# Kernel optimization log

Measured on AMD Instinct MI355X. Metric: run time of the kernel, lower is better.

The kernel has to match this reference:

```python
import jax, jax.numpy as jnp
import numpy as np

N, D, K = 100000, 512, 32
H1, H2 = 512, 256
LN2PI_2 = float(np.log(2.0 * np.pi) / 2.0)


def _glorot(key, shape):
    fan_in, fan_out = shape[0], shape[1]
    limit = np.sqrt(6.0 / (fan_in + fan_out))
    return jax.random.uniform(key, shape, jnp.float32, -limit, limit)


def setup_inputs() -> dict:
    key = jax.random.key(0)
    k0, k1, k2, k3 = jax.random.split(key, 4)
    return {
        "x": jax.random.normal(k0, (N, D), jnp.float32),
        "W1": _glorot(k1, (D, H1)),
        "b1": jnp.zeros((H1,), jnp.float32),
        "W2": _glorot(k2, (H1, H2)),
        "b2": jnp.zeros((H2,), jnp.float32),
        "W3": _glorot(k3, (H2, K)),
        "b3": jnp.zeros((K,), jnp.float32),
    }


def reference(x, W1, b1, W2, b2, W3, b3):
    # instance attention MLP: softplus hiddens, softmax output -> [N, K]
    h = jax.nn.softplus(x @ W1 + b1)
    h = jax.nn.softplus(h @ W2 + b2)
    att = jax.nn.softmax(h @ W3 + b3, axis=-1)

    att_sum = jnp.sum(att, axis=0)  # [K]
    # weighted mean: sum_n x[n,d] * att[n,k] / sum_n att[n,k]  -> [K, D]
    means = (att.T @ x) / att_sum[:, None]
    # weighted variance: E_w[x^2] - mean^2 (algebraic expansion of
    # sum_n (x - mean)^2 * att / sum att, avoids [N,K,D] intermediate)
    ex2 = (att.T @ (x * x)) / att_sum[:, None]  # [K, D]
    vars_ = ex2 - means * means

    # GMM diagonal log-likelihood, expanded to GEMM form:
    inv_v = 1.0 / vars_  # [K, D]
    maha = (x * x) @ inv_v.T - 2.0 * (x @ (means * inv_v).T) \
           + jnp.sum(means * means * inv_v, axis=-1)[None, :]  # [N, K]
    gmm_log = -0.5 * maha - 0.5 * jnp.sum(jnp.log(vars_), axis=-1)[None, :] - D * LN2PI_2
    return gmm_log, vars_
```

## Files before the change

### kernel.cpp

```cpp
#include <hip/hip_runtime.h>
#include <hip/hip_bf16.h>
#include <math.h>

#define NROWS 100000
#define DDIM  512
#define KCL   32
#define H1DIM 512
#define H2DIM 256
#define LN2PI_2 0.9189385332046727f
#define NCHUNK 196
#define NPAD  100352
#define NBLK  784

typedef __attribute__((ext_vector_type(8))) short short8;
typedef __attribute__((ext_vector_type(4))) short shortx4;
typedef __attribute__((ext_vector_type(4))) float floatx4;

__device__ __forceinline__ float softplus_f(float v) {
    return fmaxf(v, 0.f) + __logf(1.f + __expf(-fabsf(v)));
}

__device__ __forceinline__ unsigned short f2bf_rne(float f) {
    unsigned int u = __float_as_uint(f);
    return (unsigned short)((u + 0x7fffu + ((u >> 16) & 1u)) >> 16);
}

__device__ __forceinline__ float bf2f(short v) {
    return __uint_as_float(((unsigned int)(unsigned short)v) << 16);
}

__device__ __forceinline__ short8 cvt8(float4 a, float4 b) {
    union { unsigned int u[4]; short8 s; } r;
    asm("v_cvt_pk_bf16_f32 %0, %1, %2" : "=v"(r.u[0]) : "v"(a.x), "v"(a.y));
    asm("v_cvt_pk_bf16_f32 %0, %1, %2" : "=v"(r.u[1]) : "v"(a.z), "v"(a.w));
    asm("v_cvt_pk_bf16_f32 %0, %1, %2" : "=v"(r.u[2]) : "v"(b.x), "v"(b.y));
    asm("v_cvt_pk_bf16_f32 %0, %1, %2" : "=v"(r.u[3]) : "v"(b.z), "v"(b.w));
    return r.s;
}

__global__ __launch_bounds__(256) void cvt_weights(
    const float* __restrict__ W1, const float* __restrict__ W2,
    const float* __restrict__ W3, short* __restrict__ W1T,
    short* __restrict__ W2T, short* __restrict__ W3T)
{
    int idx = blockIdx.x * 256 + threadIdx.x;
    const int n1 = DDIM * H1DIM;
    const int n2 = H1DIM * H2DIM;
    const int n3 = H2DIM * KCL;
    if (idx < n1) {
        int n = idx % H1DIM, k = idx / H1DIM;
        W1T[(size_t)n * DDIM + k] = (short)f2bf_rne(W1[idx]);
    } else if (idx < n1 + n2) {
        int rel = idx - n1;
        int n = rel % H2DIM, k = rel / H2DIM;
        W2T[(size_t)n * H1DIM + k] = (short)f2bf_rne(W2[rel]);
    } else if (idx < n1 + n2 + n3) {
        int rel = idx - n1 - n2;
        int n = rel % KCL, k = rel / KCL;
        W3T[(size_t)n * H2DIM + k] = (short)f2bf_rne(W3[rel]);
    }
}

#define LDP 40
template<int AFP32>
__global__ __launch_bounds__(256) void gemm_sp(
    const void* __restrict__ Aptr, const short* __restrict__ BT,
    const float* __restrict__ bias, void* __restrict__ Cptr,
    int M, int Nc, int Kd, int out_bf16)
{
    __shared__ short As[2][128 * LDP];
    __shared__ short Bs[2][128 * LDP];

    const int tid = threadIdx.x;
    const int lid = tid & 63;
    const int w = tid >> 6;
    const int lm = lid & 15;
    const int lq = lid >> 4;
    const int wrow = (w & 1) * 64;
    const int wcol = (w >> 1) * 64;

    const int nwg = gridDim.x * gridDim.y;
    const int bid = blockIdx.y * gridDim.x + blockIdx.x;
    const int q = nwg >> 3, r = nwg & 7;
    const int xcd = bid & 7, slot = bid >> 3;
    const int L = (xcd < r ? xcd * (q + 1) : r * (q + 1) + (xcd - r) * q) + slot;
    const int row0 = (L / gridDim.x) * 128;
    const int col0 = (L % gridDim.x) * 128;

    const int sr = tid >> 2;
    const int sc = (tid & 3) << 3;

    int gr0 = row0 + sr;       if (gr0 >= M) gr0 = M - 1;
    int gr1 = row0 + 64 + sr;  if (gr1 >= M) gr1 = M - 1;

    const float* Ar0f = (const float*)Aptr + (size_t)gr0 * Kd + sc;
    const float* Ar1f = (const float*)Aptr + (size_t)gr1 * Kd + sc;
    const short* Ar0s = (const short*)Aptr + (size_t)gr0 * Kd + sc;
    const short* Ar1s = (const short*)Aptr + (size_t)gr1 * Kd + sc;
    const short* Br0 = BT + (size_t)(col0 + sr) * Kd + sc;
    const short* Br1 = BT + (size_t)(col0 + 64 + sr) * Kd + sc;

    floatx4 acc[4][4];
    #pragma unroll
    for (int i = 0; i < 4; i++)
        #pragma unroll
        for (int j = 0; j < 4; j++)
            acc[i][j] = (floatx4){0.f, 0.f, 0.f, 0.f};

    float4 fa0, fa1, fa2, fa3;
    short8 pa0, pa1, pb0, pb1;
    if constexpr (AFP32) {
        fa0 = *(const float4*)Ar0f; fa1 = *(const float4*)(Ar0f + 4);
        fa2 = *(const float4*)Ar1f; fa3 = *(const float4*)(Ar1f + 4);
    } else {
        pa0 = *(const short8*)Ar0s;
        pa1 = *(const short8*)Ar1s;
    }
    pb0 = *(const short8*)Br0;
    pb1 = *(const short8*)Br1;

    const int nk = Kd >> 5;
    for (int kt = 0; kt < nk; kt++) {
        const int buf = kt & 1;
        if constexpr (AFP32) {
            *(short8*)&As[buf][sr * LDP + sc]        = cvt8(fa0, fa1);
            *(short8*)&As[buf][(64 + sr) * LDP + sc] = cvt8(fa2, fa3);
        } else {
            *(short8*)&As[buf][sr * LDP + sc]        = pa0;
            *(short8*)&As[buf][(64 + sr) * LDP + sc] = pa1;
        }
        *(short8*)&Bs[buf][sr * LDP + sc]        = pb0;
        *(short8*)&Bs[buf][(64 + sr) * LDP + sc] = pb1;
        if (kt + 1 < nk) {
            int ko = (kt + 1) << 5;
            if constexpr (AFP32) {
                fa0 = *(const float4*)(Ar0f + ko);
                fa1 = *(const float4*)(Ar0f + ko + 4);
                fa2 = *(const float4*)(Ar1f + ko);
                fa3 = *(const float4*)(Ar1f + ko + 4);
            } else {
                pa0 = *(const short8*)(Ar0s + ko);
                pa1 = *(const short8*)(Ar1s + ko);
            }
            pb0 = *(const short8*)(Br0 + ko);
            pb1 = *(const short8*)(Br1 + ko);
        }
        __syncthreads();

        short8 a[4], b[4];
        #pragma unroll
        for (int i = 0; i < 4; i++)
            a[i] = *(const short8*)&As[buf][(wrow + i * 16 + lm) * LDP + lq * 8];
        #pragma unroll
        for (int j = 0; j < 4; j++)
            b[j] = *(const short8*)&Bs[buf][(wcol + j * 16 + lm) * LDP + lq * 8];
        #pragma unroll
        for (int i = 0; i < 4; i++)
            #pragma unroll
            for (int j = 0; j < 4; j++)
                acc[i][j] = __builtin_amdgcn_mfma_f32_16x16x32_bf16(
                    a[i], b[j], acc[i][j], 0, 0, 0);
    }

    float bb[4];
    #pragma unroll
    for (int j = 0; j < 4; j++)
        bb[j] = bias[col0 + wcol + j * 16 + lm];

    #pragma unroll
    for (int i = 0; i < 4; i++) {
        #pragma unroll
        for (int reg = 0; reg < 4; reg++) {
            int rr = row0 + wrow + i * 16 + lq * 4 + reg;
            if (rr < M) {
                #pragma unroll
                for (int j = 0; j < 4; j++) {
                    int c = col0 + wcol + j * 16 + lm;
                    float v = softplus_f(acc[i][j][reg] + bb[j]);
                    if (out_bf16)
                        ((short*)Cptr)[(size_t)rr * Nc + c] = (short)f2bf_rne(v);
                    else
                        ((float*)Cptr)[(size_t)rr * Nc + c] = v;
                }
            }
        }
    }
}

__global__ __launch_bounds__(256) void logits_mfma(
    const short* __restrict__ h2b, const short* __restrict__ W3T,
    const float* __restrict__ b3, short* __restrict__ attT,
    float* __restrict__ Patt)
{
    __shared__ short Ts[32][136];
    __shared__ float red[4][32];

    const int tid = threadIdx.x;
    const int lane = tid & 63;
    const int lm = lane & 15;
    const int lq = lane >> 4;
    const int w = tid >> 6;
    const int wrow = w * 32;
    const int row0 = blockIdx.x * 128;

    short8 bf[2][8];
    #pragma unroll
    for (int j = 0; j < 2; j++)
        #pragma unroll
        for (int s = 0; s < 8; s++)
            bf[j][s] = *(const short8*)&W3T[(j * 16 + lm) * H2DIM + s * 32 + lq * 8];

    int gr0 = row0 + wrow + lm;      if (gr0 >= NROWS) gr0 = NROWS - 1;
    int gr1 = row0 + wrow + 16 + lm; if (gr1 >= NROWS) gr1 = NROWS - 1;
    const short* a0p = h2b + (size_t)gr0 * H2DIM + lq * 8;
    const short* a1p = h2b + (size_t)gr1 * H2DIM + lq * 8;

    floatx4 acc[2][2];
    #pragma unroll
    for (int i = 0; i < 2; i++)
        #pragma unroll
        for (int j = 0; j < 2; j++)
            acc[i][j] = (floatx4){0.f, 0.f, 0.f, 0.f};

    #pragma unroll
    for (int s = 0; s < 8; s++) {
        short8 a0 = *(const short8*)(a0p + s * 32);
        short8 a1 = *(const short8*)(a1p + s * 32);
        acc[0][0] = __builtin_amdgcn_mfma_f32_16x16x32_bf16(a0, bf[0][s], acc[0][0], 0, 0, 0);
        acc[0][1] = __builtin_amdgcn_mfma_f32_16x16x32_bf16(a0, bf[1][s], acc[0][1], 0, 0, 0);
        acc[1][0] = __builtin_amdgcn_mfma_f32_16x16x32_bf16(a1, bf[0][s], acc[1][0], 0, 0, 0);
        acc[1][1] = __builtin_amdgcn_mfma_f32_16x16x32_bf16(a1, bf[1][s], acc[1][1], 0, 0, 0);
    }

    const float b3v0 = b3[lm];
    const float b3v1 = b3[16 + lm];

    float p0 = 0.f, p1 = 0.f;

    #pragma unroll
    for (int i = 0; i < 2; i++) {
        #pragma unroll
        for (int reg = 0; reg < 4; reg++) {
            const int rloc = wrow + i * 16 + lq * 4 + reg;
            const int rg = row0 + rloc;
            float v0 = acc[i][0][reg] + b3v0;
            float v1 = acc[i][1][reg] + b3v1;
            float m = fmaxf(v0, v1);
            m = fmaxf(m, __shfl_xor(m, 1));
            m = fmaxf(m, __shfl_xor(m, 2));
            m = fmaxf(m, __shfl_xor(m, 4));
            m = fmaxf(m, __shfl_xor(m, 8));
            float e0 = __expf(v0 - m);
            float e1 = __expf(v1 - m);
            float sm = e0 + e1;
            sm += __shfl_xor(sm, 1);
            sm += __shfl_xor(sm, 2);
            sm += __shfl_xor(sm, 4);
            sm += __shfl_xor(sm, 8);
            float inv = 1.f / sm;
            e0 *= inv; e1 *= inv;
            if (rg >= NROWS) { e0 = 0.f; e1 = 0.f; }
            p0 += e0; p1 += e1;
            Ts[lm][rloc]      = (short)f2bf_rne(e0);
            Ts[16 + lm][rloc] = (short)f2bf_rne(e1);
        }
    }

    p0 += __shfl_xor(p0, 16); p0 += __shfl_xor(p0, 32);
    p1 += __shfl_xor(p1, 16); p1 += __shfl_xor(p1, 32);
    if (lq == 0) { red[w][lm] = p0; red[w][16 + lm] = p1; }

    __syncthreads();

    if (tid < KCL)
        Patt[blockIdx.x * KCL + tid] =
            red[0][tid] + red[1][tid] + red[2][tid] + red[3][tid];

    #pragma unroll
    for (int p = 0; p < 2; p++) {
        int u = p * 256 + tid;
        int rr = u >> 4;
        int cs = (u & 15) << 3;
        short8 o = *(const short8*)&Ts[rr][cs];
        *(short8*)&attT[(size_t)rr * NPAD + row0 + cs] = o;
    }
}

__global__ __launch_bounds__(256, 4) void stats_mfma(
    const float* __restrict__ x, const short* __restrict__ attT,
    float* __restrict__ P)
{
    __shared__ short xT[32 * 512];

    const int tid = threadIdx.x;
    const int lane = tid & 63;
    const int lm = lane & 15;
    const int lq = lane >> 4;
    const int w = tid >> 6;
    const int kh = w >> 1;
    const int dh = w & 1;

    const int cblk = blockIdx.x;
    const int dgrp = blockIdx.y;
    const int n0 = cblk * 512;

    short8 afrag[16];
    const short* arow = attT + (size_t)(kh * 16 + lm) * NPAD + n0 + lq * 8;
    #pragma unroll
    for (int s = 0; s < 16; s++)
        afrag[s] = *(const short8*)(arow + s * 32);

    const int c = tid & 31;
    const int rq = tid >> 5;
    const bool full = (n0 + 512 <= NROWS);

    for (int dt = 0; dt < 4; dt++) {
        const int colf = dgrp * 128 + dt * 32 + c;
        __syncthreads();
        if (full) {
            const float* xp = x + (size_t)n0 * DDIM + colf;
            #pragma unroll 4
            for (int p = 0; p < 16; p++) {
                int rr = p * 32 + rq * 4;
                float f0 = xp[(size_t)(rr + 0) * DDIM];
                float f1 = xp[(size_t)(rr + 1) * DDIM];
                float f2 = xp[(size_t)(rr + 2) * DDIM];
                float f3 = xp[(size_t)(rr + 3) * DDIM];
                unsigned int u01 = (unsigned int)f2bf_rne(f0) |
                                   ((unsigned int)f2bf_rne(f1) << 16);
                unsigned int u23 = (unsigned int)f2bf_rne(f2) |
                                   ((unsigned int)f2bf_rne(f3) << 16);
                int boff = (c << 10) + ((rr * 2) ^ ((c & 15) << 4));
                *(uint2*)((char*)xT + boff) = make_uint2(u01, u23);
            }
        } else {
            #pragma unroll 4
            for (int p = 0; p < 16; p++) {
                int rr = p * 32 + rq * 4;
                int g0 = min(n0 + rr + 0, NROWS - 1);
                int g1 = min(n0 + rr + 1, NROWS - 1);
                int g2 = min(n0 + rr + 2, NROWS - 1);
                int g3 = min(n0 + rr + 3, NROWS - 1);
                float f0 = x[(size_t)g0 * DDIM + colf];
                float f1 = x[(size_t)g1 * DDIM + colf];
                float f2 = x[(size_t)g2 * DDIM + colf];
                float f3 = x[(size_t)g3 * DDIM + colf];
                unsigned int u01 = (unsigned int)f2bf_rne(f0) |
                                   ((unsigned int)f2bf_rne(f1) << 16);
                unsigned int u23 = (unsigned int)f2bf_rne(f2) |
                                   ((unsigned int)f2bf_rne(f3) << 16);
                int boff = (c << 10) + ((rr * 2) ^ ((c & 15) << 4));
                *(uint2*)((char*)xT + boff) = make_uint2(u01, u23);
            }
        }
        __syncthreads();

        floatx4 acc1 = (floatx4){0.f, 0.f, 0.f, 0.f};
        floatx4 acc2 = (floatx4){0.f, 0.f, 0.f, 0.f};
        const int rowb = (dh * 16 + lm) << 10;
        #pragma unroll
        for (int s = 0; s < 16; s++) {
            int boff = rowb + ((s * 64 + lq * 16) ^ (lm << 4));
            short8 bx = *(const short8*)((const char*)xT + boff);
            union { short8 s8; unsigned int u[4]; } bq;
            #pragma unroll
            for (int e = 0; e < 4; e++) {
                float f0 = bf2f(bx[2 * e]);
                float f1 = bf2f(bx[2 * e + 1]);
                f0 *= f0; f1 *= f1;
                bq.u[e] = (unsigned int)f2bf_rne(f0) |
                          ((unsigned int)f2bf_rne(f1) << 16);
            }
            acc1 = __builtin_amdgcn_mfma_f32_16x16x32_bf16(
                afrag[s], bx, acc1, 0, 0, 0);
            acc2 = __builtin_amdgcn_mfma_f32_16x16x32_bf16(
                afrag[s], bq.s8, acc2, 0, 0, 0);
        }

        const size_t pbase = (size_t)cblk * 32768 +
                             (size_t)(kh * 16 + lq * 4) * 512 +
                             (size_t)(dgrp * 128 + dt * 32 + dh * 16 + lm);
        #pragma unroll
        for (int reg = 0; reg < 4; reg++) {
            P[pbase + (size_t)reg * 512]         = acc1[reg];
            P[pbase + 16384 + (size_t)reg * 512] = acc2[reg];
        }
    }
}

__global__ __launch_bounds__(256) void stats_reduce(
    const float* __restrict__ P, const float* __restrict__ Patt,
    float* __restrict__ S12, float* __restrict__ att_sum)
{
    int e = blockIdx.x * 256 + threadIdx.x;
    float sum = 0.f;
    for (int cc = 0; cc < NCHUNK; cc++)
        sum += P[(size_t)cc * 32768 + e];
    S12[e] = sum;

    if (blockIdx.x == 0 && threadIdx.x < KCL) {
        float as = 0.f;
        for (int cc = 0; cc < NBLK; cc++) as += Patt[cc * KCL + threadIdx.x];
        att_sum[threadIdx.x] = as;
    }
}

__global__ __launch_bounds__(256) void finalize_stats(
    const float* __restrict__ S12, const float* __restrict__ att_sum,
    short* __restrict__ Bp, float* __restrict__ konst,
    float* __restrict__ vars_out)
{
    int k = blockIdx.x;
    int tid = threadIdx.x;
    __shared__ float red[256];

    float inv_as = 1.f / att_sum[k];
    float csum = 0.f, lsum = 0.f;
    for (int d = tid; d < DDIM; d += 256) {
        float mean = S12[k * DDIM + d] * inv_as;
        float ex2  = S12[KCL * DDIM + k * DDIM + d] * inv_as;
        float var  = ex2 - mean * mean;
        vars_out[k * DDIM + d] = var;
        float iv = 1.f / var;
        Bp[(size_t)k * 1024 + d]       = (short)f2bf_rne(-0.5f * iv);
        Bp[(size_t)k * 1024 + 512 + d] = (short)f2bf_rne(mean * iv);
        csum += mean * mean * iv;
        lsum += logf(var);
    }
    red[tid] = csum;
    __syncthreads();
    for (int s = 128; s > 0; s >>= 1) {
        if (tid < s) red[tid] += red[tid + s];
        __syncthreads();
    }
    float ctot = red[0];
    __syncthreads();
    red[tid] = lsum;
    __syncthreads();
    for (int s = 128; s > 0; s >>= 1) {
        if (tid < s) red[tid] += red[tid + s];
        __syncthreads();
    }
    if (tid == 0)
        konst[k] = -0.5f * ctot - 0.5f * red[0] - DDIM * LN2PI_2;
}

#define LDG 40
__global__ __launch_bounds__(256) void gmm_out_mfma(
    const float* __restrict__ x, const short* __restrict__ Bp,
    const float* __restrict__ konst, float* __restrict__ out)
{
    __shared__ short As_sq[256 * LDG];
    __shared__ short As_x[256 * LDG];

    const int tid = threadIdx.x;
    const int lane = tid & 63;
    const int lm = lane & 15;
    const int lq = lane >> 4;
    const int wid = tid >> 6;
    const int row0 = blockIdx.x * 256;

    floatx4 acc[4][2];
    #pragma unroll
    for (int i = 0; i < 4; i++)
        #pragma unroll
        for (int j = 0; j < 2; j++)
            acc[i][j] = (floatx4){0.f, 0.f, 0.f, 0.f};

    for (int dt = 0; dt < 16; dt++) {
        __syncthreads();
        #pragma unroll
        for (int h = 0; h < 8; h++) {
            int u = tid + h * 256;
            int rr = u >> 3;
            int seg = (u & 7) << 2;
            int gr = row0 + rr;
            float4 v = make_float4(0.f, 0.f, 0.f, 0.f);
            if (gr < NROWS)
                v = *(const float4*)&x[(size_t)gr * DDIM + dt * 32 + seg];
            shortx4 sx, sq;
            sx[0] = (short)f2bf_rne(v.x); sq[0] = (short)f2bf_rne(v.x * v.x);
            sx[1] = (short)f2bf_rne(v.y); sq[1] = (short)f2bf_rne(v.y * v.y);
            sx[2] = (short)f2bf_rne(v.z); sq[2] = (short)f2bf_rne(v.z * v.z);
            sx[3] = (short)f2bf_rne(v.w); sq[3] = (short)f2bf_rne(v.w * v.w);
            *(shortx4*)&As_x[rr * LDG + seg]  = sx;
            *(shortx4*)&As_sq[rr * LDG + seg] = sq;
        }
        __syncthreads();

        short8 a_sq[4], a_x[4], b_sq[2], b_x[2];
        #pragma unroll
        for (int i = 0; i < 4; i++) {
            int off = (wid * 64 + i * 16 + lm) * LDG + lq * 8;
            a_sq[i] = *(const short8*)&As_sq[off];
            a_x[i]  = *(const short8*)&As_x[off];
        }
        #pragma unroll
        for (int j = 0; j < 2; j++) {
            const size_t bo = (size_t)(j * 16 + lm) * 1024 + dt * 32 + lq * 8;
            b_sq[j] = *(const short8*)&Bp[bo];
            b_x[j]  = *(const short8*)&Bp[bo + 512];
        }
        #pragma unroll
        for (int i = 0; i < 4; i++)
            #pragma unroll
            for (int j = 0; j < 2; j++) {
                acc[i][j] = __builtin_amdgcn_mfma_f32_16x16x32_bf16(
                    a_sq[i], b_sq[j], acc[i][j], 0, 0, 0);
                acc[i][j] = __builtin_amdgcn_mfma_f32_16x16x32_bf16(
                    a_x[i], b_x[j], acc[i][j], 0, 0, 0);
            }
    }

    float kst[2];
    kst[0] = konst[lm];
    kst[1] = konst[16 + lm];

    #pragma unroll
    for (int i = 0; i < 4; i++) {
        #pragma unroll
        for (int reg = 0; reg < 4; reg++) {
            int rr = row0 + wid * 64 + i * 16 + lq * 4 + reg;
            if (rr < NROWS) {
                out[(size_t)rr * KCL + lm]      = acc[i][0][reg] + kst[0];
                out[(size_t)rr * KCL + 16 + lm] = acc[i][1][reg] + kst[1];
            }
        }
    }
}

extern "C" void kernel_launch(void* const* d_in, const int* in_sizes, int n_in,
                              void* d_out, int out_size, void* d_ws, size_t ws_size,
                              hipStream_t stream)
{
    const float* x  = (const float*)d_in[0];
    const float* W1 = (const float*)d_in[1];
    const float* b1 = (const float*)d_in[2];
    const float* W2 = (const float*)d_in[3];
    const float* b2 = (const float*)d_in[4];
    const float* W3 = (const float*)d_in[5];
    const float* b3 = (const float*)d_in[6];
    float* out = (float*)d_out;

    short* h1b     = (short*)d_ws;
    float* h2      = (float*)(h1b + (size_t)NROWS * H1DIM);
    float* att     = h2 + (size_t)NROWS * H2DIM;
    float* P       = att + (size_t)NROWS * KCL;
    float* PattOld = P + (size_t)NCHUNK * 32768;
    float* S12     = PattOld + NCHUNK * KCL;
    float* att_sum = S12 + 2 * KCL * DDIM;
    short* Bp      = (short*)(att_sum + KCL);
    float* konst   = (float*)(Bp + KCL * 1024);
    (void)ws_size; (void)in_sizes; (void)n_in; (void)out_size; (void)PattOld;

    short* h2b  = (short*)h2;
    short* W1T = (short*)P;
    short* W2T = W1T + H1DIM * DDIM;
    short* W3T = W2T + H2DIM * H1DIM;
    short* attT = h1b;
    float* PattN = att;

    cvt_weights<<<dim3(1568), 256, 0, stream>>>(W1, W2, W3, W1T, W2T, W3T);

    int mblocks = (NROWS + 127) / 128;

    gemm_sp<1><<<dim3(H1DIM / 128, mblocks), 256, 0, stream>>>(
        (const void*)x, W1T, b1, (void*)h1b, NROWS, H1DIM, DDIM, 1);
    gemm_sp<0><<<dim3(H2DIM / 128, mblocks), 256, 0, stream>>>(
        (const void*)h1b, W2T, b2, (void*)h2b, NROWS, H2DIM, H1DIM, 1);
    logits_mfma<<<dim3(NBLK), 256, 0, stream>>>(h2b, W3T, b3, attT, PattN);
    stats_mfma<<<dim3(NCHUNK, 4), 256, 0, stream>>>(x, attT, P);
    stats_reduce<<<dim3(128), 256, 0, stream>>>(P, PattN, S12, att_sum);
    finalize_stats<<<dim3(KCL), 256, 0, stream>>>(
        S12, att_sum, Bp, konst, out + (size_t)NROWS * KCL);
    gmm_out_mfma<<<dim3((NROWS + 255) / 256), 256, 0, stream>>>(x, Bp, konst, out);
}
```

Measured before the change: 658.4 us.

## Pre-convert x to bf16 for first GEMM and prefetch x tiles in gmm_out

Result: no change. 652.6 us (-0.9%).

```diff
diff --git a/kernel.cpp b/kernel.cpp
--- a/kernel.cpp
+++ b/kernel.cpp
@@ -29,13 +29,18 @@
     return __uint_as_float(((unsigned int)(unsigned short)v) << 16);
 }
 
-__device__ __forceinline__ short8 cvt8(float4 a, float4 b) {
-    union { unsigned int u[4]; short8 s; } r;
-    asm("v_cvt_pk_bf16_f32 %0, %1, %2" : "=v"(r.u[0]) : "v"(a.x), "v"(a.y));
-    asm("v_cvt_pk_bf16_f32 %0, %1, %2" : "=v"(r.u[1]) : "v"(a.z), "v"(a.w));
-    asm("v_cvt_pk_bf16_f32 %0, %1, %2" : "=v"(r.u[2]) : "v"(b.x), "v"(b.y));
-    asm("v_cvt_pk_bf16_f32 %0, %1, %2" : "=v"(r.u[3]) : "v"(b.z), "v"(b.w));
-    return r.s;
+__global__ __launch_bounds__(256) void cvt_x_bf16(
+    const float* __restrict__ x, short* __restrict__ xb)
+{
+    size_t i = ((size_t)blockIdx.x * 256 + threadIdx.x) * 8;
+    float4 f0 = *(const float4*)&x[i];
+    float4 f1 = *(const float4*)&x[i + 4];
+    short8 o;
+    o[0] = (short)f2bf_rne(f0.x); o[1] = (short)f2bf_rne(f0.y);
+    o[2] = (short)f2bf_rne(f0.z); o[3] = (short)f2bf_rne(f0.w);
+    o[4] = (short)f2bf_rne(f1.x); o[5] = (short)f2bf_rne(f1.y);
+    o[6] = (short)f2bf_rne(f1.z); o[7] = (short)f2bf_rne(f1.w);
+    *(short8*)&xb[i] = o;
 }
 
 __global__ __launch_bounds__(256) void cvt_weights(
@@ -62,9 +67,8 @@
 }
 
 #define LDP 40
-template<int AFP32>
 __global__ __launch_bounds__(256) void gemm_sp(
-    const void* __restrict__ Aptr, const short* __restrict__ BT,
+    const short* __restrict__ A, const short* __restrict__ BT,
     const float* __restrict__ bias, void* __restrict__ Cptr,
     int M, int Nc, int Kd, int out_bf16)
 {
@@ -92,11 +96,8 @@
 
     int gr0 = row0 + sr;       if (gr0 >= M) gr0 = M - 1;
     int gr1 = row0 + 64 + sr;  if (gr1 >= M) gr1 = M - 1;
-
-    const float* Ar0f = (const float*)Aptr + (size_t)gr0 * Kd + sc;
-    const float* Ar1f = (const float*)Aptr + (size_t)gr1 * Kd + sc;
-    const short* Ar0s = (const short*)Aptr + (size_t)gr0 * Kd + sc;
-    const short* Ar1s = (const short*)Aptr + (size_t)gr1 * Kd + sc;
+    const short* Ar0 = A + (size_t)gr0 * Kd + sc;
+    const short* Ar1 = A + (size_t)gr1 * Kd + sc;
     const short* Br0 = BT + (size_t)(col0 + sr) * Kd + sc;
     const short* Br1 = BT + (size_t)(col0 + 64 + sr) * Kd + sc;
 
@@ -107,41 +108,23 @@
         for (int j = 0; j < 4; j++)
             acc[i][j] = (floatx4){0.f, 0.f, 0.f, 0.f};
 
-    float4 fa0, fa1, fa2, fa3;
     short8 pa0, pa1, pb0, pb1;
-    if constexpr (AFP32) {
-        fa0 = *(const float4*)Ar0f; fa1 = *(const float4*)(Ar0f + 4);
-        fa2 = *(const float4*)Ar1f; fa3 = *(const float4*)(Ar1f + 4);
-    } else {
-        pa0 = *(const short8*)Ar0s;
-        pa1 = *(const short8*)Ar1s;
-    }
+    pa0 = *(const short8*)Ar0;
+    pa1 = *(const short8*)Ar1;
     pb0 = *(const short8*)Br0;
     pb1 = *(const short8*)Br1;
 
     const int nk = Kd >> 5;
     for (int kt = 0; kt < nk; kt++) {
         const int buf = kt & 1;
-        if constexpr (AFP32) {
-            *(short8*)&As[buf][sr * LDP + sc]        = cvt8(fa0, fa1);
-            *(short8*)&As[buf][(64 + sr) * LDP + sc] = cvt8(fa2, fa3);
-        } else {
-            *(short8*)&As[buf][sr * LDP + sc]        = pa0;
-            *(short8*)&As[buf][(64 + sr) * LDP + sc] = pa1;
-        }
+        *(short8*)&As[buf][sr * LDP + sc]        = pa0;
+        *(short8*)&As[buf][(64 + sr) * LDP + sc] = pa1;
         *(short8*)&Bs[buf][sr * LDP + sc]        = pb0;
         *(short8*)&Bs[buf][(64 + sr) * LDP + sc] = pb1;
         if (kt + 1 < nk) {
             int ko = (kt + 1) << 5;
-            if constexpr (AFP32) {
-                fa0 = *(const float4*)(Ar0f + ko);
-                fa1 = *(const float4*)(Ar0f + ko + 4);
-                fa2 = *(const float4*)(Ar1f + ko);
-                fa3 = *(const float4*)(Ar1f + ko + 4);
-            } else {
-                pa0 = *(const short8*)(Ar0s + ko);
-                pa1 = *(const short8*)(Ar1s + ko);
-            }
+            pa0 = *(const short8*)(Ar0 + ko);
+            pa1 = *(const short8*)(Ar1 + ko);
             pb0 = *(const short8*)(Br0 + ko);
             pb1 = *(const short8*)(Br1 + ko);
         }
@@ -467,24 +450,48 @@
         for (int j = 0; j < 2; j++)
             acc[i][j] = (floatx4){0.f, 0.f, 0.f, 0.f};
 
+    int rrh[8], segh[8], grh[8];
+    bool okh[8];
+    #pragma unroll
+    for (int h = 0; h < 8; h++) {
+        int u = tid + h * 256;
+        rrh[h] = u >> 3;
+        segh[h] = (u & 7) << 2;
+        int gr = row0 + rrh[h];
+        okh[h] = (gr < NROWS);
+        grh[h] = okh[h] ? gr : 0;
+    }
+
+    float4 pf[8];
+    #pragma unroll
+    for (int h = 0; h < 8; h++) {
+        float4 v = make_float4(0.f, 0.f, 0.f, 0.f);
+        if (okh[h]) v = *(const float4*)&x[(size_t)grh[h] * DDIM + segh[h]];
+        pf[h] = v;
+    }
+
     for (int dt = 0; dt < 16; dt++) {
         __syncthreads();
         #pragma unroll
         for (int h = 0; h < 8; h++) {
-            int u = tid + h * 256;
-            int rr = u >> 3;
-            int seg = (u & 7) << 2;
-            int gr = row0 + rr;
-            float4 v = make_float4(0.f, 0.f, 0.f, 0.f);
-            if (gr < NROWS)
-                v = *(const float4*)&x[(size_t)gr * DDIM + dt * 32 + seg];
+            float4 v = pf[h];
             shortx4 sx, sq;
             sx[0] = (short)f2bf_rne(v.x); sq[0] = (short)f2bf_rne(v.x * v.x);
             sx[1] = (short)f2bf_rne(v.y); sq[1] = (short)f2bf_rne(v.y * v.y);
             sx[2] = (short)f2bf_rne(v.z); sq[2] = (short)f2bf_rne(v.z * v.z);
             sx[3] = (short)f2bf_rne(v.w); sq[3] = (short)f2bf_rne(v.w * v.w);
-            *(shortx4*)&As_x[rr * LDG + seg]  = sx;
-            *(shortx4*)&As_sq[rr * LDG + seg] = sq;
+            *(shortx4*)&As_x[rrh[h] * LDG + segh[h]]  = sx;
+            *(shortx4*)&As_sq[rrh[h] * LDG + segh[h]] = sq;
+        }
+        if (dt + 1 < 16) {
+            #pragma unroll
+            for (int h = 0; h < 8; h++) {
+                float4 v = make_float4(0.f, 0.f, 0.f, 0.f);
+                if (okh[h])
+                    v = *(const float4*)&x[(size_t)grh[h] * DDIM +
+                                           (dt + 1) * 32 + segh[h]];
+                pf[h] = v;
+            }
         }
         __syncthreads();
 
@@ -553,6 +560,7 @@
     float* konst   = (float*)(Bp + KCL * 1024);
     (void)ws_size; (void)in_sizes; (void)n_in; (void)out_size; (void)PattOld;
 
+    short* xb   = (short*)h2;
     short* h2b  = (short*)h2;
     short* W1T = (short*)P;
     short* W2T = W1T + H1DIM * DDIM;
@@ -560,14 +568,15 @@
     short* attT = h1b;
     float* PattN = att;
 
+    cvt_x_bf16<<<dim3(NROWS * DDIM / 2048), 256, 0, stream>>>(x, xb);
     cvt_weights<<<dim3(1568), 256, 0, stream>>>(W1, W2, W3, W1T, W2T, W3T);
 
     int mblocks = (NROWS + 127) / 128;
 
-    gemm_sp<1><<<dim3(H1DIM / 128, mblocks), 256, 0, stream>>>(
-        (const void*)x, W1T, b1, (void*)h1b, NROWS, H1DIM, DDIM, 1);
-    gemm_sp<0><<<dim3(H2DIM / 128, mblocks), 256, 0, stream>>>(
-        (const void*)h1b, W2T, b2, (void*)h2b, NROWS, H2DIM, H1DIM, 1);
+    gemm_sp<<<dim3(H1DIM / 128, mblocks), 256, 0, stream>>>(
+        xb, W1T, b1, (void*)h1b, NROWS, H1DIM, DDIM, 1);
+    gemm_sp<<<dim3(H2DIM / 128, mblocks), 256, 0, stream>>>(
+        h1b, W2T, b2, (void*)h2b, NROWS, H2DIM, H1DIM, 1);
     logits_mfma<<<dim3(NBLK), 256, 0, stream>>>(h2b, W3T, b3, attT, PattN);
     stats_mfma<<<dim3(NCHUNK, 4), 256, 0, stream>>>(x, attT, P);
     stats_reduce<<<dim3(128), 256, 0, stream>>>(P, PattN, S12, att_sum);
```
